# Performance work log

Hardware: AMD Instinct MI355X
Metric: run time of the kernel (lower is better)

The kernel has to match this reference:

```python
import jax, jax.numpy as jnp
import numpy as np
from jax import lax

B, G, D, S = 1, 2048, 64, 2
H_FULL = 200
H0 = H_FULL // 2 ** (S - 1)
PC_RANGE = (-50.0, -50.0, -4.0, 50.0, 50.0, 4.0)
THRESH = 0.05
CHUNK = 128


def conv3x3(x, w):
    # x: [b,c,h,w], w: [o,i,3,3]
    return lax.conv_general_dilated(x, w, (1, 1), 'SAME',
                                    dimension_numbers=('NCHW', 'OIHW', 'NCHW'))


def instance_norm(x, eps=1e-5):
    mu = x.mean(axis=(2, 3), keepdims=True)
    var = x.var(axis=(2, 3), keepdims=True)
    return (x - mu) / jnp.sqrt(var + eps)


def basic_block(x, w1, w2):
    # conv-(BN@init=identity)-relu-conv-(BN)-add-relu
    h = jax.nn.relu(conv3x3(x, w1))
    h = conv3x3(h, w2)
    return jax.nn.relu(x + h)


def upsampling_add(x, skip, w):
    b, c, h, wd = x.shape
    xu = jax.image.resize(x, (b, c, 2 * h, 2 * wd), method='bilinear')
    xu = instance_norm(conv3x3(xu, w))
    return xu + skip


def render_stage(means, cov6, feats, opac, mask, H, W):
    # Orthographic BEV splatting (3DGS-style EWA + front-to-back compositing).
    g, d = feats.shape
    sh = H / 100.0
    sw = W / 100.0
    # full_proj_transform: px = -sh*y + H/2 ; py = -sw*x + W/2
    u = -sh * means[:, 1] + 0.5 * H
    v = -sw * means[:, 0] + 0.5 * W
    # cov2d = J Sigma J^T + 0.3*I, J = [[0,-sh,0],[-sw,0,0]]
    a = sh * sh * cov6[:, 3] + 0.3
    c = sw * sw * cov6[:, 0] + 0.3
    bb = sh * sw * cov6[:, 1]
    det = jnp.maximum(a * c - bb * bb, 1e-8)
    A = c / det
    Bc = -bb / det
    C = a / det
    xs = jnp.arange(W, dtype=jnp.float32)
    ys = jnp.arange(H, dtype=jnp.float32)
    nc = g // CHUNK

    def step(carry, inp):
        T, out = carry
        u_, v_, A_, B_, C_, op_, mk_, ft_ = inp
        dx = u_[:, None, None] - xs[None, None, :]
        dy = v_[:, None, None] - ys[None, :, None]
        power = (-0.5 * (A_[:, None, None] * dx * dx + C_[:, None, None] * dy * dy)
                 - B_[:, None, None] * dx * dy)
        alpha = jnp.minimum(op_[:, None, None] * jnp.exp(power), 0.99)
        alpha = jnp.where((alpha >= 1.0 / 255.0) & mk_[:, None, None] & (power <= 0.0),
                          alpha, 0.0)
        cp = jnp.cumprod(1.0 - alpha, axis=0)
        t_exc = jnp.concatenate([jnp.ones_like(cp[:1]), cp[:-1]], 0) * T
        out = out + jnp.einsum('ghw,gd->dhw', alpha * t_exc, ft_)
        return (T * cp[-1], out), None

    ch = lambda arr: arr.reshape(nc, CHUNK, *arr.shape[1:])
    init = (jnp.ones((H, W), jnp.float32), jnp.zeros((d, H, W), jnp.float32))
    (_, out), _ = lax.scan(step, init,
                           (ch(u), ch(v), ch(A), ch(Bc), ch(C), ch(opac), ch(mask), ch(feats)))
    return out  # bg color = 0


def setup_inputs() -> dict:
    key = jax.random.key(0)
    ks = jax.random.split(key, 10)
    features = jax.random.normal(ks[0], (B, G, D), jnp.float32)
    xy = jax.random.uniform(ks[1], (B, G, 2), jnp.float32, -55.0, 55.0)
    z = jax.random.uniform(ks[2], (B, G, 1), jnp.float32, -5.0, 5.0)
    means3D = jnp.concatenate([xy, z], -1)
    L = jax.random.normal(ks[3], (B, G, 3, 3), jnp.float32) * 0.5
    Sig = jnp.einsum('bgij,bgkj->bgik', L, L) + 0.1 * jnp.eye(3, dtype=jnp.float32)
    cov3D = jnp.stack([Sig[..., 0, 0], Sig[..., 0, 1], Sig[..., 0, 2],
                       Sig[..., 1, 1], Sig[..., 1, 2], Sig[..., 2, 2]], -1)
    opacities = jax.random.uniform(ks[4], (B, G, S), jnp.float32)
    w_scale = 1.0 / np.sqrt(D * 9)
    bev_emb = jax.random.normal(ks[5], (H0 * H0, D), jnp.float32) * 0.02
    conv1_w = jax.random.normal(ks[6], (S, D, D, 3, 3), jnp.float32) * w_scale
    blk_w = jax.random.normal(ks[7], (S, 2, 2, D, D, 3, 3), jnp.float32) * w_scale
    up_w = jax.random.normal(ks[8], (S - 1, D, D, 3, 3), jnp.float32) * w_scale
    return {'features': features, 'means3D': means3D, 'cov3D': cov3D,
            'opacities': opacities, 'bev_emb': bev_emb, 'conv1_w': conv1_w,
            'blk_w': blk_w, 'up_w': up_w}


def reference(features, means3D, cov3D, opacities, bev_emb, conv1_w, blk_w, up_w):
    b = features.shape[0]
    d = features.shape[-1]
    m = means3D
    mask_pos = ((m[..., 0] >= PC_RANGE[0]) & (m[..., 0] <= PC_RANGE[3]) &
                (m[..., 1] >= PC_RANGE[1]) & (m[..., 1] <= PC_RANGE[4]) &
                (m[..., 2] >= PC_RANGE[2]) & (m[..., 2] <= PC_RANGE[5]))
    num_g = jnp.float32(0.0)
    bevs = []
    for s in range(S):
        H = H0 * 2 ** s
        mask = (opacities[..., s] > THRESH) & mask_pos
        rend = jax.vmap(lambda mn, cv, ft, op, mk: render_stage(mn, cv, ft, op, mk, H, H))
        bevs.append(rend(means3D, cov3D, features, opacities[..., s], mask))
        num_g = num_g + jnp.mean(jnp.sum(mask.astype(jnp.float32), 1))
    x = jnp.broadcast_to(jnp.transpose(bev_emb.reshape(H0, H0, d), (2, 0, 1))[None],
                         (b, d, H0, H0))
    for s in range(S):
        bev = conv3x3(bevs[s], conv1_w[s])
        if s == 0:
            x = x + bev
        else:
            x = upsampling_add(x, bev, up_w[s - 1])
        for blk in range(2):
            x = basic_block(x, blk_w[s, blk, 0], blk_w[s, blk, 1])
    return x, num_g
```

## Files before the change

kernel.cpp:

```cpp
#include <hip/hip_runtime.h>
#include <math.h>

#define G_N 2048
#define CCH 256
#define PSTR 12
#define NBLK 1024
#define WC (64 * 64 * 9)

typedef short bhalf8 __attribute__((ext_vector_type(8)));
typedef float f32x4 __attribute__((ext_vector_type(4)));
typedef unsigned short u16;

__device__ __forceinline__ u16 f2bf(float f) {
    unsigned u = __float_as_uint(f);
    unsigned r = (u + 0x7fffu + ((u >> 16) & 1u)) >> 16;
    return (u16)r;
}
__device__ __forceinline__ float b2f(u16 h) {
    return __uint_as_float((unsigned)h << 16);
}

__device__ __forceinline__ void chstore4(u16* p, ushort4 v) {
    union { unsigned long long u; ushort4 s; } x; x.s = v;
    __hip_atomic_store((unsigned long long*)p, x.u,
                       __ATOMIC_RELAXED, __HIP_MEMORY_SCOPE_AGENT);
}
__device__ __forceinline__ void cstore8(float* p, float a, float b) {
    union { unsigned long long u; float f[2]; } x;
    x.f[0] = a; x.f[1] = b;
    __hip_atomic_store((unsigned long long*)p, x.u,
                       __ATOMIC_RELAXED, __HIP_MEMORY_SCOPE_AGENT);
}
__device__ __forceinline__ float cload(const float* p) {
    return __hip_atomic_load(p, __ATOMIC_RELAXED, __HIP_MEMORY_SCOPE_AGENT);
}
__device__ __forceinline__ int iload(const int* p) {
    return __hip_atomic_load(p, __ATOMIC_RELAXED, __HIP_MEMORY_SCOPE_AGENT);
}

__device__ __forceinline__ void gbar(int* leaf, int* root, int* flag, int phase) {
    asm volatile("s_waitcnt vmcnt(0) lgkmcnt(0)" ::: "memory");
    __syncthreads();
    if (threadIdx.x == 0) {
        int g = blockIdx.x >> 5;
        int old = atomicAdd(&leaf[g * 16], 1);
        if ((old & 31) == 31) {
            int o2 = atomicAdd(root, 1);
            if ((o2 & 31) == 31)
                __hip_atomic_store(flag, phase, __ATOMIC_RELAXED,
                                   __HIP_MEMORY_SCOPE_AGENT);
        }
        while (__hip_atomic_load(flag, __ATOMIC_RELAXED,
                                 __HIP_MEMORY_SCOPE_AGENT) < phase)
            __builtin_amdgcn_s_sleep(16);
    }
    __syncthreads();
    asm volatile("" ::: "memory");
}

__device__ __forceinline__ void render_tile(
    int unit, const float* __restrict__ params,
    const float* __restrict__ feats, u16* __restrict__ out0,
    u16* __restrict__ out1, char* smem)
{
    int s = (unit < 169) ? 0 : 1;
    int t = (s == 0) ? unit : unit - 169;
    int tw = (s == 0) ? 13 : 25;
    int bxx = t % tw, byy = t / tw;
    int H = 100 << s;
    const float* P = params + s * G_N * PSTR;
    u16* out = s ? out1 : out0;

    float* raw = (float*)smem;
    float* cmp = raw + CCH * PSTR;
    int* s_wsum = (int*)(smem + 24576);

    int tid = threadIdx.x;
    int w = tid >> 6, lane = tid & 63;
    int x0 = bxx * 8, y0 = byy * 8;
    int px = x0 + (lane & 7), py = y0 + (lane >> 3);
    bool active = (px < H) && (py < H);
    float fx = (float)px, fy = (float)py;
    float tx0 = (float)x0, tx1 = (float)min(H - 1, x0 + 7);
    float ty0 = (float)y0, ty1 = (float)min(H - 1, y0 + 7);

    f32x4 acc[4];
#pragma unroll
    for (int k = 0; k < 4; ++k) acc[k] = (f32x4){0.f, 0.f, 0.f, 0.f};
    float T = 1.f;

    for (int base = 0; base < G_N; base += CCH) {
        int anyalive = __syncthreads_or((int)(active && T > 1e-6f));
        if (!anyalive) break;
        for (int i = tid; i < CCH * 3; i += 256)
            ((float4*)raw)[i] = ((const float4*)(P + base * PSTR))[i];
        __syncthreads();
        float u = raw[tid * PSTR + 0], v = raw[tid * PSTR + 1];
        float rx = raw[tid * PSTR + 8], ry = raw[tid * PSTR + 9];
        bool pass = (u + rx >= tx0) && (u - rx <= tx1) &&
                    (v + ry >= ty0) && (v - ry <= ty1);
        unsigned long long bal = __ballot(pass);
        int prefix = __popcll(bal & ((1ull << lane) - 1ull));
        if (lane == 0) s_wsum[w] = __popcll(bal);
        __syncthreads();
        int woff = 0;
        for (int k = 0; k < 4; ++k) if (k < w) woff += s_wsum[k];
        if (pass) {
            float4* dst = (float4*)(cmp + (woff + prefix) * PSTR);
            const float4* src = (const float4*)(raw + tid * PSTR);
            dst[0] = src[0]; dst[1] = src[1]; dst[2] = src[2];
        }
        __syncthreads();
        int nc = s_wsum[0] + s_wsum[1] + s_wsum[2] + s_wsum[3];
        if (active && T > 1e-6f) {
            for (int j = 0; j < nc; ++j) {
                float4 q0 = *(const float4*)(cmp + j * PSTR);
                float4 q1 = *(const float4*)(cmp + j * PSTR + 4);
                float dx = q0.x - fx, dy = q0.y - fy;
                float power = -0.5f * (q0.z * dx * dx + q1.x * dy * dy) - q0.w * dx * dy;
                if (power <= 0.f && power >= q1.z) {
                    float alpha = fminf(q1.y * __expf(power), 0.99f);
                    float wgt = alpha * T;
                    const f32x4* f4 = (const f32x4*)(feats + __float_as_int(q1.w) * 64) + w * 4;
#pragma unroll
                    for (int k = 0; k < 4; ++k) {
                        f32x4 fv = f4[k];
                        acc[k][0] = fmaf(wgt, fv[0], acc[k][0]);
                        acc[k][1] = fmaf(wgt, fv[1], acc[k][1]);
                        acc[k][2] = fmaf(wgt, fv[2], acc[k][2]);
                        acc[k][3] = fmaf(wgt, fv[3], acc[k][3]);
                    }
                    T *= (1.f - alpha);
                }
            }
        }
    }

    __syncthreads();
    float* shf = (float*)smem;
#pragma unroll
    for (int k = 0; k < 4; ++k)
        *(float4*)&shf[lane * 68 + w * 16 + k * 4] =
            (float4){acc[k][0], acc[k][1], acc[k][2], acc[k][3]};
    __syncthreads();
    for (int j = tid; j < 1024; j += 256) {
        int lp = j >> 4, c4 = (j & 15) * 4;
        int gy = y0 + (lp >> 3), gx = x0 + (lp & 7);
        if (gy < H && gx < H) {
            float4 v = *(float4*)&shf[lp * 68 + c4];
            ushort4 o = { f2bf(v.x), f2bf(v.y), f2bf(v.z), f2bf(v.w) };
            chstore4(&out[((gy * H + gx) << 6) + c4], o);
        }
    }
}

__device__ __forceinline__ void conv_tile(
    int bx, int H, const u16* __restrict__ in, const u16* __restrict__ wp,
    const float* __restrict__ bev, u16* __restrict__ outb,
    int ups, int dostats, float* __restrict__ sacc, char* smem)
{
    u16* xlds = (u16*)smem;
    u16* fin  = (u16*)(smem + 14400);
    float* red = (float*)(smem + 25600);

    int tid = threadIdx.x;
    int gw = (H + 7) >> 3;
    int by = bx / gw, bxx = bx - by * gw;
    int y0 = by * 8, x0 = bxx * 8;
    int w = tid >> 6, lane = tid & 63;
    int n = lane & 15, q = lane >> 4;
    int Hh = H >> 1;
    int oy = (y0 >> 1) - 2, ox = (x0 >> 1) - 2;

    if (ups) {
        for (int i = tid; i < 512; i += 256) {
            int px = i >> 3, c8 = (i & 7) * 8;
            int iy = px >> 3, ix = px & 7;
            int gyi = oy + iy, gxi = ox + ix;
            uint4 v = {0, 0, 0, 0};
            if (gyi >= 0 && gyi < Hh && gxi >= 0 && gxi < Hh)
                v = *(const uint4*)&in[((gyi * Hh + gxi) << 6) + c8];
            *(uint4*)&fin[px * 72 + c8] = v;
        }
        __syncthreads();
        for (int i = tid; i < 1600; i += 256) {
            int px = i >> 4, c4 = (i & 15) * 4;
            int yy = px / 10, xx = px - yy * 10;
            int gy = y0 - 1 + yy, gx = x0 - 1 + xx;
            ushort4 v = {0, 0, 0, 0};
            if (gy >= 0 && gy < H && gx >= 0 && gx < H) {
                int yi = gy >> 1, xi = gx >> 1;
                int yb = (gy & 1) ? min(yi + 1, Hh - 1) : max(yi - 1, 0);
                int xb = (gx & 1) ? min(xi + 1, Hh - 1) : max(xi - 1, 0);
                int t0 = yi - oy, t1 = xi - ox, t2 = yb - oy, t3 = xb - ox;
                ushort4 f00 = *(const ushort4*)&fin[(t0 * 8 + t1) * 72 + c4];
                ushort4 f01 = *(const ushort4*)&fin[(t0 * 8 + t3) * 72 + c4];
                ushort4 f10 = *(const ushort4*)&fin[(t2 * 8 + t1) * 72 + c4];
                ushort4 f11 = *(const ushort4*)&fin[(t2 * 8 + t3) * 72 + c4];
                v.x = f2bf(0.5625f * b2f(f00.x) + 0.1875f * (b2f(f01.x) + b2f(f10.x)) + 0.0625f * b2f(f11.x));
                v.y = f2bf(0.5625f * b2f(f00.y) + 0.1875f * (b2f(f01.y) + b2f(f10.y)) + 0.0625f * b2f(f11.y));
                v.z = f2bf(0.5625f * b2f(f00.z) + 0.1875f * (b2f(f01.z) + b2f(f10.z)) + 0.0625f * b2f(f11.z));
                v.w = f2bf(0.5625f * b2f(f00.w) + 0.1875f * (b2f(f01.w) + b2f(f10.w)) + 0.0625f * b2f(f11.w));
            }
            *(ushort4*)&xlds[px * 72 + c4] = v;
        }
    } else {
        for (int i = tid; i < 800; i += 256) {
            int px = i >> 3, c8 = (i & 7) * 8;
            int yy = px / 10, xx = px - yy * 10;
            int gy = y0 - 1 + yy, gx = x0 - 1 + xx;
            uint4 v = {0, 0, 0, 0};
            if (gy >= 0 && gy < H && gx >= 0 && gx < H)
                v = *(const uint4*)&in[((gy * H + gx) << 6) + c8];
            *(uint4*)&xlds[px * 72 + c8] = v;
        }
    }
    __syncthreads();

    f32x4 acc[4];
#pragma unroll
    for (int m = 0; m < 4; ++m) acc[m] = (f32x4){0.f, 0.f, 0.f, 0.f};
    const bhalf8* wp8 = (const bhalf8*)wp;
    int sy = 2 * w + (n >> 3), sx = n & 7;

    bhalf8 a0 = wp8[0 * 64 + lane];
    bhalf8 a1 = wp8[1 * 64 + lane];
    bhalf8 a2 = wp8[2 * 64 + lane];
    bhalf8 a3 = wp8[3 * 64 + lane];
    bhalf8 bb = *(const bhalf8*)&xlds[(sy * 10 + sx) * 72 + q * 8];

#pragma unroll 1
    for (int p = 0; p < 18; ++p) {
        bhalf8 na0, na1, na2, na3, nbb;
        if (p < 17) {
            int pn = p + 1;
            na0 = wp8[(pn * 4 + 0) * 64 + lane];
            na1 = wp8[(pn * 4 + 1) * 64 + lane];
            na2 = wp8[(pn * 4 + 2) * 64 + lane];
            na3 = wp8[(pn * 4 + 3) * 64 + lane];
            int tap = pn >> 1, ch = pn & 1;
            int dy = tap / 3, dx = tap - dy * 3;
            nbb = *(const bhalf8*)&xlds[((sy + dy) * 10 + sx + dx) * 72 + ch * 32 + q * 8];
        }
        acc[0] = __builtin_amdgcn_mfma_f32_16x16x32_bf16(a0, bb, acc[0], 0, 0, 0);
        acc[1] = __builtin_amdgcn_mfma_f32_16x16x32_bf16(a1, bb, acc[1], 0, 0, 0);
        acc[2] = __builtin_amdgcn_mfma_f32_16x16x32_bf16(a2, bb, acc[2], 0, 0, 0);
        acc[3] = __builtin_amdgcn_mfma_f32_16x16x32_bf16(a3, bb, acc[3], 0, 0, 0);
        a0 = na0; a1 = na1; a2 = na2; a3 = na3; bb = nbb;
    }

    int gy = y0 + sy, gx = x0 + sx;
    if (gy < H && gx < H) {
        int base = (gy * H + gx) << 6;
#pragma unroll
        for (int m = 0; m < 4; ++m) {
            int oc0 = m * 16 + q * 4;
            float v0 = acc[m][0], v1 = acc[m][1], v2 = acc[m][2], v3 = acc[m][3];
            if (bev) {
                float4 av = *(const float4*)&bev[base + oc0];
                v0 += av.x; v1 += av.y; v2 += av.z; v3 += av.w;
            }
            ushort4 o = { f2bf(v0), f2bf(v1), f2bf(v2), f2bf(v3) };
            chstore4(&outb[base + oc0], o);
        }
    }

    if (dostats) {
#pragma unroll
        for (int m = 0; m < 4; ++m)
#pragma unroll
            for (int r = 0; r < 4; ++r) {
                float v = acc[m][r];
                float s = v, s2 = v * v;
#pragma unroll
                for (int d = 1; d < 16; d <<= 1) {
                    s += __shfl_xor(s, d, 64);
                    s2 += __shfl_xor(s2, d, 64);
                }
                if (n == 0) {
                    int oc = m * 16 + q * 4 + r;
                    red[w * 128 + oc] = s;
                    red[w * 128 + 64 + oc] = s2;
                }
            }
        __syncthreads();
        if (tid < 128) {
            float t = red[tid] + red[128 + tid] + red[256 + tid] + red[384 + tid];
            atomicAdd(&sacc[tid], t);
        }
    }
}

__device__ __forceinline__ void bb_tile(
    int bx, int H, const u16* __restrict__ in,
    const u16* __restrict__ wp1, const u16* __restrict__ wp2,
    u16* __restrict__ outb, float* __restrict__ outf, int final_,
    int nrm, const u16* __restrict__ nskip, const float* __restrict__ sraw,
    char* smem)
{
    u16* xin  = (u16*)smem;
    u16* ilds = (u16*)(smem + 20736);
    float* nm = (float*)(smem + 35136);
    float* nr = nm + 64;

    int tid = threadIdx.x;
    int gw = (H + 7) >> 3;
    int by = bx / gw, bxx = bx - by * gw;
    int y0 = by * 8, x0 = bxx * 8;
    int w = tid >> 6, lane = tid & 63;
    int n = lane & 15, q = lane >> 4;

    if (nrm) {
        if (tid < 64) {
            float s = cload(&sraw[tid]), s2 = cload(&sraw[64 + tid]);
            float mean = s * (1.f / 40000.f);
            float var = s2 * (1.f / 40000.f) - mean * mean;
            nm[tid] = mean;
            nr[tid] = rsqrtf(var + 1e-5f);
        }
        __syncthreads();
        for (int i = tid; i < 2304; i += 256) {
            int px = i >> 4, c4 = (i & 15) * 4;
            int yy = px / 12, xx = px - yy * 12;
            int gy = y0 - 2 + yy, gx = x0 - 2 + xx;
            ushort4 v = {0, 0, 0, 0};
            if (gy >= 0 && gy < H && gx >= 0 && gx < H) {
                int off = ((gy * H + gx) << 6) + c4;
                ushort4 a = *(const ushort4*)&in[off];
                ushort4 b = *(const ushort4*)&nskip[off];
                v.x = f2bf((b2f(a.x) - nm[c4 + 0]) * nr[c4 + 0] + b2f(b.x));
                v.y = f2bf((b2f(a.y) - nm[c4 + 1]) * nr[c4 + 1] + b2f(b.y));
                v.z = f2bf((b2f(a.z) - nm[c4 + 2]) * nr[c4 + 2] + b2f(b.z));
                v.w = f2bf((b2f(a.w) - nm[c4 + 3]) * nr[c4 + 3] + b2f(b.w));
            }
            *(ushort4*)&xin[px * 72 + c4] = v;
        }
    } else {
        for (int i = tid; i < 1152; i += 256) {
            int px = i >> 3, c8 = (i & 7) * 8;
            int yy = px / 12, xx = px - yy * 12;
            int gy = y0 - 2 + yy, gx = x0 - 2 + xx;
            uint4 v = {0, 0, 0, 0};
            if (gy >= 0 && gy < H && gx >= 0 && gx < H)
                v = *(const uint4*)&in[((gy * H + gx) << 6) + c8];
            *(uint4*)&xin[px * 72 + c8] = v;
        }
    }
    __syncthreads();

#pragma unroll 1
    for (int r = 0; r < 2; ++r) {
        int t = w + 4 * r;
        int px = t * 16 + n;
        bool val = px < 100;
        int pc = val ? px : 0;
        int yy = pc / 10, xx = pc - yy * 10;

        f32x4 acc1[4];
#pragma unroll
        for (int m = 0; m < 4; ++m) acc1[m] = (f32x4){0.f, 0.f, 0.f, 0.f};

        {
            const bhalf8* wp8_ = (const bhalf8*)wp1;
            bhalf8 a0 = wp8_[0 * 64 + lane];
            bhalf8 a1 = wp8_[1 * 64 + lane];
            bhalf8 a2 = wp8_[2 * 64 + lane];
            bhalf8 a3 = wp8_[3 * 64 + lane];
            bhalf8 bb = *(const bhalf8*)&xin[(yy * 12 + xx) * 72 + q * 8];
#pragma unroll 1
            for (int p = 0; p < 18; ++p) {
                bhalf8 na0, na1, na2, na3, nbb;
                if (p < 17) {
                    int pn = p + 1;
                    na0 = wp8_[(pn * 4 + 0) * 64 + lane];
                    na1 = wp8_[(pn * 4 + 1) * 64 + lane];
                    na2 = wp8_[(pn * 4 + 2) * 64 + lane];
                    na3 = wp8_[(pn * 4 + 3) * 64 + lane];
                    int tap = pn >> 1, ch = pn & 1;
                    int dy = tap / 3, dx = tap - dy * 3;
                    nbb = *(const bhalf8*)&xin[((yy + dy) * 12 + xx + dx) * 72 + ch * 32 + q * 8];
                }
                acc1[0] = __builtin_amdgcn_mfma_f32_16x16x32_bf16(a0, bb, acc1[0], 0, 0, 0);
                acc1[1] = __builtin_amdgcn_mfma_f32_16x16x32_bf16(a1, bb, acc1[1], 0, 0, 0);
                acc1[2] = __builtin_amdgcn_mfma_f32_16x16x32_bf16(a2, bb, acc1[2], 0, 0, 0);
                acc1[3] = __builtin_amdgcn_mfma_f32_16x16x32_bf16(a3, bb, acc1[3], 0, 0, 0);
                a0 = na0; a1 = na1; a2 = na2; a3 = na3; bb = nbb;
            }
        }

        int iy = y0 - 1 + yy, ix = x0 - 1 + xx;
        bool ok1 = val && iy >= 0 && iy < H && ix >= 0 && ix < H;
        if (val) {
#pragma unroll
            for (int m = 0; m < 4; ++m) {
                ushort4 o = {0, 0, 0, 0};
                if (ok1) {
                    o.x = f2bf(fmaxf(acc1[m][0], 0.f));
                    o.y = f2bf(fmaxf(acc1[m][1], 0.f));
                    o.z = f2bf(fmaxf(acc1[m][2], 0.f));
                    o.w = f2bf(fmaxf(acc1[m][3], 0.f));
                }
                *(ushort4*)&ilds[px * 72 + m * 16 + q * 4] = o;
            }
        }
    }
    __syncthreads();

    f32x4 acc[4];
#pragma unroll
    for (int m = 0; m < 4; ++m) acc[m] = (f32x4){0.f, 0.f, 0.f, 0.f};
    const bhalf8* w2 = (const bhalf8*)wp2;
    int sy = 2 * w + (n >> 3), sx = n & 7;

    bhalf8 a0 = w2[0 * 64 + lane];
    bhalf8 a1 = w2[1 * 64 + lane];
    bhalf8 a2 = w2[2 * 64 + lane];
    bhalf8 a3 = w2[3 * 64 + lane];
    bhalf8 bb = *(const bhalf8*)&ilds[(sy * 10 + sx) * 72 + q * 8];

#pragma unroll 1
    for (int p = 0; p < 18; ++p) {
        bhalf8 na0, na1, na2, na3, nbb;
        if (p < 17) {
            int pn = p + 1;
            na0 = w2[(pn * 4 + 0) * 64 + lane];
            na1 = w2[(pn * 4 + 1) * 64 + lane];
            na2 = w2[(pn * 4 + 2) * 64 + lane];
            na3 = w2[(pn * 4 + 3) * 64 + lane];
            int tap = pn >> 1, ch = pn & 1;
            int dy = tap / 3, dx = tap - dy * 3;
            nbb = *(const bhalf8*)&ilds[((sy + dy) * 10 + sx + dx) * 72 + ch * 32 + q * 8];
        }
        acc[0] = __builtin_amdgcn_mfma_f32_16x16x32_bf16(a0, bb, acc[0], 0, 0, 0);
        acc[1] = __builtin_amdgcn_mfma_f32_16x16x32_bf16(a1, bb, acc[1], 0, 0, 0);
        acc[2] = __builtin_amdgcn_mfma_f32_16x16x32_bf16(a2, bb, acc[2], 0, 0, 0);
        acc[3] = __builtin_amdgcn_mfma_f32_16x16x32_bf16(a3, bb, acc[3], 0, 0, 0);
        a0 = na0; a1 = na1; a2 = na2; a3 = na3; bb = nbb;
    }

    int gy = y0 + sy, gx = x0 + sx;
    if (gy < H && gx < H) {
        int base = (gy * H + gx) << 6;
#pragma unroll
        for (int m = 0; m < 4; ++m) {
            int oc0 = m * 16 + q * 4;
            ushort4 xr = *(const ushort4*)&xin[((sy + 2) * 12 + sx + 2) * 72 + oc0];
            float v0 = fmaxf(acc[m][0] + b2f(xr.x), 0.f);
            float v1 = fmaxf(acc[m][1] + b2f(xr.y), 0.f);
            float v2 = fmaxf(acc[m][2] + b2f(xr.z), 0.f);
            float v3 = fmaxf(acc[m][3] + b2f(xr.w), 0.f);
            if (final_) {
                int pix = gy * H + gx;
                outf[(oc0 + 0) * H * H + pix] = v0;
                outf[(oc0 + 1) * H * H + pix] = v1;
                outf[(oc0 + 2) * H * H + pix] = v2;
                outf[(oc0 + 3) * H * H + pix] = v3;
            } else {
                ushort4 o = { f2bf(v0), f2bf(v1), f2bf(v2), f2bf(v3) };
                chstore4(&outb[base + oc0], o);
            }
        }
    }
}

__global__ __launch_bounds__(256, 4) void gls_mega(
    const float* __restrict__ feats, const float* __restrict__ bev_emb,
    const float* __restrict__ conv1_w, const float* __restrict__ blk_w,
    const float* __restrict__ up_w, const float* __restrict__ means,
    const float* __restrict__ cov6, const float* __restrict__ opac,
    u16* __restrict__ wprep, float* __restrict__ params, int* __restrict__ cnts,
    u16* __restrict__ R0h, u16* __restrict__ X0h,
    u16* __restrict__ X1h, u16* __restrict__ X2h,
    u16* __restrict__ Qr0h, u16* __restrict__ Sh,
    u16* __restrict__ Uh, u16* __restrict__ Y1h,
    float* __restrict__ out, int* __restrict__ barmem, float* __restrict__ sacc)
{
    __shared__ __align__(16) char smem[36352];
    int bid = blockIdx.x;
    int tid = threadIdx.x;
    int* leaf = barmem;
    int* root = barmem + 512;
    int* flag = barmem + 513;
    int ph = 0;

    if (bid < 16) {
        int item = bid * 256 + tid;
        int s = item >> 11, g = item & 2047;
        float mx = means[g * 3 + 0], my = means[g * 3 + 1], mz = means[g * 3 + 2];
        float op = opac[g * 2 + s];
        bool mask = (mx >= -50.f && mx <= 50.f && my >= -50.f && my <= 50.f &&
                     mz >= -4.f && mz <= 4.f && op > 0.05f);
        float Hs = (float)(100 << s), sh = (float)(1 << s);
        float u = 0.f, v = 0.f, A = 0.f, B = 0.f, C = 0.f, pthr = 0.f;
        float rx = -1.f, ry = -1.f;
        if (mask) {
            u = -sh * my + 0.5f * Hs;
            v = -sh * mx + 0.5f * Hs;
            float a = sh * sh * cov6[g * 6 + 3] + 0.3f;
            float c = sh * sh * cov6[g * 6 + 0] + 0.3f;
            float bb = sh * sh * cov6[g * 6 + 1];
            float det = fmaxf(a * c - bb * bb, 1e-8f);
            float t = logf(255.f * op);
            A = c / det; B = -bb / det; C = a / det;
            pthr = -t;
            rx = sqrtf(2.f * t * a); ry = sqrtf(2.f * t * c);
        }
        float* Q = params + (s * G_N + g) * PSTR;
        cstore8(&Q[0], u, v);
        cstore8(&Q[2], A, B);
        cstore8(&Q[4], C, op);
        cstore8(&Q[6], pthr, __int_as_float(g));
        cstore8(&Q[8], rx, ry);
        unsigned long long bal = __ballot(mask);
        if ((tid & 63) == 0) atomicAdd(&cnts[s], __popcll(bal));
    }
    gbar(leaf, root, flag, ++ph);

    if (bid < 794) {
        render_tile(bid, params, feats, R0h, Qr0h, smem);
    } else if (bid < 992) {
        int rb = bid - 794;
        int p = rb % 18, c = rb / 18;
        const float* src;
        if (c == 0) src = conv1_w;
        else if (c <= 4) src = blk_w + (c - 1) * WC;
        else if (c == 5) src = conv1_w + WC;
        else if (c == 6) src = up_w;
        else src = blk_w + (c - 3) * WC;
        int tap = p >> 1;
        int m = tid >> 6, lane = tid & 63;
        int oc = m * 16 + (lane & 15);
        int ci0 = (p & 1) * 32 + (lane >> 4) * 8;
        u16 v[8];
#pragma unroll
        for (int j = 0; j < 8; ++j)
            v[j] = f2bf(src[(oc * 64 + ci0 + j) * 9 + tap]);
        u16* dst = wprep + ((c * 18 + p) * 4 + m) * 64 * 8 + lane * 8;
        chstore4(dst, (ushort4){v[0], v[1], v[2], v[3]});
        chstore4(dst + 4, (ushort4){v[4], v[5], v[6], v[7]});
    }
    gbar(leaf, root, flag, ++ph);

    if (bid < 169)
        conv_tile(bid, 100, R0h, wprep + 0 * WC, bev_emb, X0h, 0, 0, nullptr, smem);
    gbar(leaf, root, flag, ++ph);

    if (bid < 169)
        bb_tile(bid, 100, X0h, wprep + 1 * WC, wprep + 2 * WC, X1h,
                nullptr, 0, 0, nullptr, nullptr, smem);
    else if (bid < 481)
        conv_tile(bid - 169, 200, Qr0h, wprep + 5 * WC, nullptr, Sh, 0, 0, nullptr, smem);
    gbar(leaf, root, flag, ++ph);

    if (bid < 169)
        bb_tile(bid, 100, X1h, wprep + 3 * WC, wprep + 4 * WC, X2h,
                nullptr, 0, 0, nullptr, nullptr, smem);
    else if (bid < 482)
        conv_tile(312 + bid - 169, 200, Qr0h, wprep + 5 * WC, nullptr, Sh, 0, 0, nullptr, smem);
    gbar(leaf, root, flag, ++ph);

    if (bid < 625)
        conv_tile(bid, 200, X2h, wprep + 6 * WC, nullptr, Uh, 1, 1, sacc, smem);
    gbar(leaf, root, flag, ++ph);

    if (bid < 625)
        bb_tile(bid, 200, Uh, wprep + 7 * WC, wprep + 8 * WC, Y1h,
                nullptr, 0, 1, Sh, sacc, smem);
    gbar(leaf, root, flag, ++ph);

    if (bid == 0 && threadIdx.x == 0)
        out[2560000] = (float)(iload(&cnts[0]) + iload(&cnts[1]));
    if (bid < 625)
        bb_tile(bid, 200, Y1h, wprep + 9 * WC, wprep + 10 * WC, nullptr,
                out, 1, 0, nullptr, nullptr, smem);
}

extern "C" void kernel_launch(void* const* d_in, const int* in_sizes, int n_in,
                              void* d_out, int out_size, void* d_ws, size_t ws_size,
                              hipStream_t stream)
{
    const float* feats   = (const float*)d_in[0];
    const float* means   = (const float*)d_in[1];
    const float* cov6    = (const float*)d_in[2];
    const float* opac    = (const float*)d_in[3];
    const float* bev_emb = (const float*)d_in[4];
    const float* conv1_w = (const float*)d_in[5];
    const float* blk_w   = (const float*)d_in[6];
    const float* up_w    = (const float*)d_in[7];
    float* out = (float*)d_out;
    float* ws = (float*)d_ws;

    float* P      = ws;
    int*   cnts   = (int*)(ws + 49152);
    int*   barmem = (int*)(ws + 49280);
    float* sacc   = ws + 49856;
    u16*   wprep  = (u16*)(ws + 50176);

    u16* R0h  = (u16*)(ws + 262144);
    u16* X0h  = (u16*)(ws + 589824);
    u16* X1h  = (u16*)(ws + 917504);
    u16* X2h  = (u16*)(ws + 1245184);
    u16* Qr0h = (u16*)(ws + 1572864);
    u16* Sh   = (u16*)(ws + 2883584);
    u16* Uh   = (u16*)(ws + 4194304);
    u16* Y1h  = (u16*)(ws + 5505024);

    hipMemsetAsync(cnts, 0, (49984 - 49152) * 4, stream);
    gls_mega<<<NBLK, 256, 0, stream>>>(feats, bev_emb, conv1_w, blk_w, up_w,
                                       means, cov6, opac, wprep, P, cnts,
                                       R0h, X0h, X1h, X2h, Qr0h, Sh, Uh, Y1h,
                                       out, barmem, sacc);
    (void)in_sizes; (void)n_in; (void)out_size; (void)ws_size;
}
```

Baseline: 259.9 us.

## Replace grid-wide barriers with dataflow job queue using per-tile dependency flags

Result: slower. 362.0 us (+39.3%).

```diff
diff --git a/kernel.cpp b/kernel.cpp
--- a/kernel.cpp
+++ b/kernel.cpp
@@ -6,6 +6,7 @@
 #define PSTR 12
 #define NBLK 1024
 #define WC (64 * 64 * 9)
+#define NJOBS 4015
 
 typedef short bhalf8 __attribute__((ext_vector_type(8)));
 typedef float f32x4 __attribute__((ext_vector_type(4)));
@@ -38,21 +39,35 @@
     return __hip_atomic_load(p, __ATOMIC_RELAXED, __HIP_MEMORY_SCOPE_AGENT);
 }
 
-__device__ __forceinline__ void gbar(int* leaf, int* root, int* flag, int phase) {
+__device__ __forceinline__ void publish_flag(int* f) {
     asm volatile("s_waitcnt vmcnt(0) lgkmcnt(0)" ::: "memory");
     __syncthreads();
+    if (threadIdx.x == 0)
+        __hip_atomic_store(f, 1, __ATOMIC_RELAXED, __HIP_MEMORY_SCOPE_AGENT);
+}
+__device__ __forceinline__ void publish_ctr(int* c) {
+    asm volatile("s_waitcnt vmcnt(0) lgkmcnt(0)" ::: "memory");
+    __syncthreads();
+    if (threadIdx.x == 0) atomicAdd(c, 1);
+}
+__device__ __forceinline__ void wait_ctr(int* c, int n) {
+    __syncthreads();
+    if (threadIdx.x == 0)
+        while (iload(c) < n) __builtin_amdgcn_s_sleep(8);
+    __syncthreads();
+    asm volatile("" ::: "memory");
+}
+__device__ __forceinline__ void wait_tiles(int* flags, int tw, int t) {
+    __syncthreads();
     if (threadIdx.x == 0) {
-        int g = blockIdx.x >> 5;
-        int old = atomicAdd(&leaf[g * 16], 1);
-        if ((old & 31) == 31) {
-            int o2 = atomicAdd(root, 1);
-            if ((o2 & 31) == 31)
-                __hip_atomic_store(flag, phase, __ATOMIC_RELAXED,
-                                   __HIP_MEMORY_SCOPE_AGENT);
-        }
-        while (__hip_atomic_load(flag, __ATOMIC_RELAXED,
-                                 __HIP_MEMORY_SCOPE_AGENT) < phase)
-            __builtin_amdgcn_s_sleep(16);
+        int by = t / tw, bx = t - by * tw;
+        for (int dy = -1; dy <= 1; ++dy)
+            for (int dx = -1; dx <= 1; ++dx) {
+                int ny = by + dy, nx = bx + dx;
+                if (ny < 0 || ny >= tw || nx < 0 || nx >= tw) continue;
+                int* f = &flags[ny * tw + nx];
+                while (iload(f) == 0) __builtin_amdgcn_s_sleep(8);
+            }
     }
     __syncthreads();
     asm volatile("" ::: "memory");
@@ -468,111 +483,136 @@
     const float* __restrict__ conv1_w, const float* __restrict__ blk_w,
     const float* __restrict__ up_w, const float* __restrict__ means,
     const float* __restrict__ cov6, const float* __restrict__ opac,
-    u16* __restrict__ wprep, float* __restrict__ params, int* __restrict__ cnts,
+    u16* __restrict__ wprep, float* __restrict__ params, int* __restrict__ F,
     u16* __restrict__ R0h, u16* __restrict__ X0h,
     u16* __restrict__ X1h, u16* __restrict__ X2h,
     u16* __restrict__ Qr0h, u16* __restrict__ Sh,
     u16* __restrict__ Uh, u16* __restrict__ Y1h,
-    float* __restrict__ out, int* __restrict__ barmem, float* __restrict__ sacc)
+    float* __restrict__ out, float* __restrict__ sacc)
 {
     __shared__ __align__(16) char smem[36352];
     int bid = blockIdx.x;
     int tid = threadIdx.x;
-    int* leaf = barmem;
-    int* root = barmem + 512;
-    int* flag = barmem + 513;
-    int ph = 0;
-
-    if (bid < 16) {
-        int item = bid * 256 + tid;
-        int s = item >> 11, g = item & 2047;
-        float mx = means[g * 3 + 0], my = means[g * 3 + 1], mz = means[g * 3 + 2];
-        float op = opac[g * 2 + s];
-        bool mask = (mx >= -50.f && mx <= 50.f && my >= -50.f && my <= 50.f &&
-                     mz >= -4.f && mz <= 4.f && op > 0.05f);
-        float Hs = (float)(100 << s), sh = (float)(1 << s);
-        float u = 0.f, v = 0.f, A = 0.f, B = 0.f, C = 0.f, pthr = 0.f;
-        float rx = -1.f, ry = -1.f;
-        if (mask) {
-            u = -sh * my + 0.5f * Hs;
-            v = -sh * mx + 0.5f * Hs;
-            float a = sh * sh * cov6[g * 6 + 3] + 0.3f;
-            float c = sh * sh * cov6[g * 6 + 0] + 0.3f;
-            float bb = sh * sh * cov6[g * 6 + 1];
-            float det = fmaxf(a * c - bb * bb, 1e-8f);
-            float t = logf(255.f * op);
-            A = c / det; B = -bb / det; C = a / det;
-            pthr = -t;
-            rx = sqrtf(2.f * t * a); ry = sqrtf(2.f * t * c);
-        }
-        float* Q = params + (s * G_N + g) * PSTR;
-        cstore8(&Q[0], u, v);
-        cstore8(&Q[2], A, B);
-        cstore8(&Q[4], C, op);
-        cstore8(&Q[6], pthr, __int_as_float(g));
-        cstore8(&Q[8], rx, ry);
-        unsigned long long bal = __ballot(mask);
-        if ((tid & 63) == 0) atomicAdd(&cnts[s], __popcll(bal));
-    }
-    gbar(leaf, root, flag, ++ph);
-
-    if (bid < 794) {
-        render_tile(bid, params, feats, R0h, Qr0h, smem);
-    } else if (bid < 992) {
-        int rb = bid - 794;
-        int p = rb % 18, c = rb / 18;
-        const float* src;
-        if (c == 0) src = conv1_w;
-        else if (c <= 4) src = blk_w + (c - 1) * WC;
-        else if (c == 5) src = conv1_w + WC;
-        else if (c == 6) src = up_w;
-        else src = blk_w + (c - 3) * WC;
-        int tap = p >> 1;
-        int m = tid >> 6, lane = tid & 63;
-        int oc = m * 16 + (lane & 15);
-        int ci0 = (p & 1) * 32 + (lane >> 4) * 8;
-        u16 v[8];
-#pragma unroll
-        for (int j = 0; j < 8; ++j)
-            v[j] = f2bf(src[(oc * 64 + ci0 + j) * 9 + tap]);
-        u16* dst = wprep + ((c * 18 + p) * 4 + m) * 64 * 8 + lane * 8;
-        chstore4(dst, (ushort4){v[0], v[1], v[2], v[3]});
-        chstore4(dst + 4, (ushort4){v[4], v[5], v[6], v[7]});
-    }
-    gbar(leaf, root, flag, ++ph);
-
-    if (bid < 169)
-        conv_tile(bid, 100, R0h, wprep + 0 * WC, bev_emb, X0h, 0, 0, nullptr, smem);
-    gbar(leaf, root, flag, ++ph);
-
-    if (bid < 169)
-        bb_tile(bid, 100, X0h, wprep + 1 * WC, wprep + 2 * WC, X1h,
-                nullptr, 0, 0, nullptr, nullptr, smem);
-    else if (bid < 481)
-        conv_tile(bid - 169, 200, Qr0h, wprep + 5 * WC, nullptr, Sh, 0, 0, nullptr, smem);
-    gbar(leaf, root, flag, ++ph);
-
-    if (bid < 169)
-        bb_tile(bid, 100, X1h, wprep + 3 * WC, wprep + 4 * WC, X2h,
-                nullptr, 0, 0, nullptr, nullptr, smem);
-    else if (bid < 482)
-        conv_tile(312 + bid - 169, 200, Qr0h, wprep + 5 * WC, nullptr, Sh, 0, 0, nullptr, smem);
-    gbar(leaf, root, flag, ++ph);
-
-    if (bid < 625)
-        conv_tile(bid, 200, X2h, wprep + 6 * WC, nullptr, Uh, 1, 1, sacc, smem);
-    gbar(leaf, root, flag, ++ph);
-
-    if (bid < 625)
-        bb_tile(bid, 200, Uh, wprep + 7 * WC, wprep + 8 * WC, Y1h,
-                nullptr, 0, 1, Sh, sacc, smem);
-    gbar(leaf, root, flag, ++ph);
-
-    if (bid == 0 && threadIdx.x == 0)
-        out[2560000] = (float)(iload(&cnts[0]) + iload(&cnts[1]));
-    if (bid < 625)
-        bb_tile(bid, 200, Y1h, wprep + 9 * WC, wprep + 10 * WC, nullptr,
-                out, 1, 0, nullptr, nullptr, smem);
+    int* rf0 = F + 16;
+    int* rf1 = F + 192;
+    int* xf0 = F + 832;
+    int* xf1 = F + 1008;
+    int* yf  = F + 1184;
+
+    for (int rnd = 0; rnd < 4; ++rnd) {
+        int job = rnd * NBLK + bid;
+        if (job >= NJOBS) return;
+
+        if (job < 16) {
+            int item = job * 256 + tid;
+            int s = item >> 11, g = item & 2047;
+            float mx = means[g * 3 + 0], my = means[g * 3 + 1], mz = means[g * 3 + 2];
+            float op = opac[g * 2 + s];
+            bool mask = (mx >= -50.f && mx <= 50.f && my >= -50.f && my <= 50.f &&
+                         mz >= -4.f && mz <= 4.f && op > 0.05f);
+            float Hs = (float)(100 << s), sh = (float)(1 << s);
+            float u = 0.f, v = 0.f, A = 0.f, B = 0.f, C = 0.f, pthr = 0.f;
+            float rx = -1.f, ry = -1.f;
+            if (mask) {
+                u = -sh * my + 0.5f * Hs;
+                v = -sh * mx + 0.5f * Hs;
+                float a = sh * sh * cov6[g * 6 + 3] + 0.3f;
+                float c = sh * sh * cov6[g * 6 + 0] + 0.3f;
+                float bb = sh * sh * cov6[g * 6 + 1];
+                float det = fmaxf(a * c - bb * bb, 1e-8f);
+                float t = logf(255.f * op);
+                A = c / det; B = -bb / det; C = a / det;
+                pthr = -t;
+                rx = sqrtf(2.f * t * a); ry = sqrtf(2.f * t * c);
+            }
+            float* Q = params + (s * G_N + g) * PSTR;
+            cstore8(&Q[0], u, v);
+            cstore8(&Q[2], A, B);
+            cstore8(&Q[4], C, op);
+            cstore8(&Q[6], pthr, __int_as_float(g));
+            cstore8(&Q[8], rx, ry);
+            unsigned long long bal = __ballot(mask);
+            if ((tid & 63) == 0) atomicAdd(&F[s], __popcll(bal));
+            publish_ctr(&F[2]);
+            if (job == 0 && tid == 0) {
+                while (iload(&F[2]) < 16) __builtin_amdgcn_s_sleep(8);
+                out[2560000] = (float)(iload(&F[0]) + iload(&F[1]));
+            }
+        } else if (job < 214) {
+            int rb = job - 16;
+            int p = rb % 18, c = rb / 18;
+            const float* src;
+            if (c == 0) src = conv1_w;
+            else if (c <= 4) src = blk_w + (c - 1) * WC;
+            else if (c == 5) src = conv1_w + WC;
+            else if (c == 6) src = up_w;
+            else src = blk_w + (c - 3) * WC;
+            int tap = p >> 1;
+            int m = tid >> 6, lane = tid & 63;
+            int oc = m * 16 + (lane & 15);
+            int ci0 = (p & 1) * 32 + (lane >> 4) * 8;
+            u16 v[8];
+#pragma unroll
+            for (int j = 0; j < 8; ++j)
+                v[j] = f2bf(src[(oc * 64 + ci0 + j) * 9 + tap]);
+            u16* dst = wprep + ((c * 18 + p) * 4 + m) * 64 * 8 + lane * 8;
+            chstore4(dst, (ushort4){v[0], v[1], v[2], v[3]});
+            chstore4(dst + 4, (ushort4){v[4], v[5], v[6], v[7]});
+            publish_ctr(&F[3]);
+        } else if (job < 383) {
+            int t = job - 214;
+            wait_ctr(&F[2], 16);
+            render_tile(t, params, feats, R0h, Qr0h, smem);
+            publish_flag(&rf0[t]);
+        } else if (job < 1008) {
+            int t = job - 383;
+            wait_ctr(&F[2], 16);
+            render_tile(169 + t, params, feats, R0h, Qr0h, smem);
+            publish_flag(&rf1[t]);
+        } else if (job < 1177) {
+            int t = job - 1008;
+            wait_ctr(&F[3], 198);
+            wait_tiles(rf0, 13, t);
+            conv_tile(t, 100, R0h, wprep + 0 * WC, bev_emb, X0h, 0, 0, nullptr, smem);
+            publish_flag(&xf0[t]);
+        } else if (job < 1802) {
+            int t = job - 1177;
+            wait_ctr(&F[3], 198);
+            wait_tiles(rf1, 25, t);
+            conv_tile(t, 200, Qr0h, wprep + 5 * WC, nullptr, Sh, 0, 0, nullptr, smem);
+            publish_ctr(&F[5]);
+        } else if (job < 1971) {
+            int t = job - 1802;
+            wait_tiles(xf0, 13, t);
+            bb_tile(t, 100, X0h, wprep + 1 * WC, wprep + 2 * WC, X1h,
+                    nullptr, 0, 0, nullptr, nullptr, smem);
+            publish_flag(&xf1[t]);
+        } else if (job < 2140) {
+            int t = job - 1971;
+            wait_tiles(xf1, 13, t);
+            bb_tile(t, 100, X1h, wprep + 3 * WC, wprep + 4 * WC, X2h,
+                    nullptr, 0, 0, nullptr, nullptr, smem);
+            publish_ctr(&F[4]);
+        } else if (job < 2765) {
+            int t = job - 2140;
+            wait_ctr(&F[4], 169);
+            conv_tile(t, 200, X2h, wprep + 6 * WC, nullptr, Uh, 1, 1, sacc, smem);
+            publish_ctr(&F[6]);
+        } else if (job < 3390) {
+            int t = job - 2765;
+            wait_ctr(&F[6], 625);
+            wait_ctr(&F[5], 625);
+            bb_tile(t, 200, Uh, wprep + 7 * WC, wprep + 8 * WC, Y1h,
+                    nullptr, 0, 1, Sh, sacc, smem);
+            publish_flag(&yf[t]);
+        } else {
+            int t = job - 3390;
+            wait_tiles(yf, 25, t);
+            bb_tile(t, 200, Y1h, wprep + 9 * WC, wprep + 10 * WC, nullptr,
+                    out, 1, 0, nullptr, nullptr, smem);
+        }
+        __syncthreads();
+    }
 }
 
 extern "C" void kernel_launch(void* const* d_in, const int* in_sizes, int n_in,
@@ -590,11 +630,10 @@
     float* out = (float*)d_out;
     float* ws = (float*)d_ws;
 
-    float* P      = ws;
-    int*   cnts   = (int*)(ws + 49152);
-    int*   barmem = (int*)(ws + 49280);
-    float* sacc   = ws + 49856;
-    u16*   wprep  = (u16*)(ws + 50176);
+    float* P     = ws;
+    int*   F     = (int*)(ws + 49152);
+    float* sacc  = ws + 51200;
+    u16*   wprep = (u16*)(ws + 51456);
 
     u16* R0h  = (u16*)(ws + 262144);
     u16* X0h  = (u16*)(ws + 589824);
@@ -605,10 +644,10 @@
     u16* Uh   = (u16*)(ws + 4194304);
     u16* Y1h  = (u16*)(ws + 5505024);
 
-    hipMemsetAsync(cnts, 0, (49984 - 49152) * 4, stream);
+    hipMemsetAsync(F, 0, (2048 + 128) * 4, stream);
     gls_mega<<<NBLK, 256, 0, stream>>>(feats, bev_emb, conv1_w, blk_w, up_w,
-                                       means, cov6, opac, wprep, P, cnts,
+                                       means, cov6, opac, wprep, P, F,
                                        R0h, X0h, X1h, X2h, Qr0h, Sh, Uh, Y1h,
-                                       out, barmem, sacc);
+                                       out, sacc);
     (void)in_sizes; (void)n_in; (void)out_size; (void)ws_size;
 }
```
